# Optimization experiments

Hardware: AMD Instinct MI355X
Metric: run time of the kernel (lower is better)

## Reference

```python
import jax, jax.numpy as jnp
import numpy as np

N_SPK, M_UTT, D_EMB = 8192, 10, 128
CLAMP_MIN = 1e-6


def setup_inputs() -> dict:
    key = jax.random.key(0)
    x = jax.random.normal(key, (N_SPK, M_UTT, D_EMB), dtype=jnp.float32)
    w = jnp.asarray(10.0, dtype=jnp.float32)   # learned scale (init_w)
    b = jnp.asarray(-5.0, dtype=jnp.float32)   # learned bias  (init_b)
    return {"x": x, "w": w, "b": b}


def reference(x, w, b):
    # x: [N, M, D]. Faithful to the torch module:
    #   - centroids = mean over all M utterances per speaker
    #   - calc_new_centroids replaces speaker's own centroid with mean(dvecs[spkr,:M]),
    #     which IS the full centroid -> new_centroids == centroids (no-op, kept faithful)
    #   - only the last utterance (utt_indx == M-1) contributes a row -> [N, 1, N]
    n, m, d = x.shape
    centroids = jnp.mean(x, axis=1)                       # [N, D]
    last = x[:, m - 1, :]                                 # [N, D] last utterance per speaker
    num = jnp.einsum('nd,kd->nk', last, centroids)        # [N, N]
    denom = (jnp.linalg.norm(last, axis=1)[:, None]
             * jnp.linalg.norm(centroids, axis=1)[None, :])
    cos_sim = jnp.clip(num / denom, CLAMP_MIN)            # torch.clamp(x, 1e-6) = min-clamp
    logits = cos_sim * w + b                              # [N, N] (view(-1, N) with M=1)
    # CrossEntropyLoss with labels arange(N) (repeat_interleave with M=1 is identity)
    logp = jax.nn.log_softmax(logits, axis=-1)
    labels = jnp.arange(n)
    loss = -jnp.mean(jnp.take_along_axis(logp, labels[:, None], axis=1))
    return loss
```

## Files before the change

### kernel.cpp

```cpp
#include <hip/hip_runtime.h>
#include <hip/hip_bf16.h>


typedef __attribute__((ext_vector_type(8))) short short8;
typedef __attribute__((ext_vector_type(4))) float f32x4;

#define NSPK 8192
#define DEMB 128
#define MUTT 10
#define LOG2E 1.44269504088896340736f
#define LN2   0.69314718055994530942f

#define WS_ZDIAG 0
#define WS_ZSUM  8192
#define WS_LASTB 65536
#define WS_CENTB 2162688

__global__ __launch_bounds__(256) void k1_prep(const float* __restrict__ x,
                                               const float* __restrict__ wp,
                                               float* __restrict__ W,
                                               __hip_bfloat16* __restrict__ lastb,
                                               __hip_bfloat16* __restrict__ centb) {
    const int wv = threadIdx.x >> 6;
    const int l  = threadIdx.x & 63;
    const int n  = blockIdx.x * 4 + wv;
    if (blockIdx.x < 32) W[WS_ZSUM + blockIdx.x * 256 + threadIdx.x] = 0.f;

    const float* xr = x + (size_t)n * (MUTT * DEMB) + 2 * l;
    float sx = 0.f, sy = 0.f, vx = 0.f, vy = 0.f;
#pragma unroll
    for (int m = 0; m < MUTT; ++m) {
        float2 t = *(const float2*)(xr + m * DEMB);
        vx = t.x; vy = t.y; sx += t.x; sy += t.y;
    }
    const float cx = sx * 0.1f, cy = sy * 0.1f;
    float sl = vx * vx + vy * vy;
    float sc = cx * cx + cy * cy;
    float dp = vx * cx + vy * cy;
#pragma unroll
    for (int off = 1; off < 64; off <<= 1) {
        sl += __shfl_xor(sl, off);
        sc += __shfl_xor(sc, off);
        dp += __shfl_xor(dp, off);
    }
    const float il = rsqrtf(sl), ic = rsqrtf(sc);
    const float scale = wp[0] * LOG2E;
    const float as = il * scale;
    __hip_bfloat162 lv, cv;
    lv.x = __float2bfloat16(vx * as); lv.y = __float2bfloat16(vy * as);
    cv.x = __float2bfloat16(cx * ic); cv.y = __float2bfloat16(cy * ic);
    *(__hip_bfloat162*)(lastb + n * DEMB + 2 * l) = lv;
    *(__hip_bfloat162*)(centb + n * DEMB + 2 * l) = cv;
    if (l == 0) {
        const float lo = scale >= 0.f ? 1e-6f * scale : -INFINITY;
        const float hi = scale >= 0.f ? INFINITY : 1e-6f * scale;
        W[WS_ZDIAG + n] = fminf(fmaxf(dp * il * ic * scale, lo), hi);
    }
}

__global__ __launch_bounds__(256, 2) void k2_main(
        const __hip_bfloat16* __restrict__ lastb,
        const __hip_bfloat16* __restrict__ centb,
        const float* __restrict__ wp,
        float* __restrict__ W) {
    const int tid  = threadIdx.x;
    const int lane = tid & 63;
    const int wv   = tid >> 6;
    const int quad = lane >> 4;
    const int l16  = lane & 15;
    const int R0   = blockIdx.x * 256;
    const int C0   = blockIdx.y * 512;
    const float scale = wp[0] * LOG2E;
    const float lo = scale >= 0.f ? 1e-6f * scale : -INFINITY;
    const float hi = scale >= 0.f ? INFINITY : 1e-6f * scale;

    __shared__ uint4 Bs4[1024];
    char* Bsc = (char*)Bs4;

    short8 a[4][4];
    {
        const short* ap = (const short*)lastb + (size_t)(R0 + wv * 64 + l16) * DEMB + quad * 8;
#pragma unroll
        for (int rt = 0; rt < 4; ++rt)
#pragma unroll
            for (int kc = 0; kc < 4; ++kc)
                a[rt][kc] = *(const short8*)(ap + rt * 16 * DEMB + kc * 32);
    }

    int roff[4];
#pragma unroll
    for (int kc = 0; kc < 4; ++kc)
        roff[kc] = l16 * 256 + (((quad + 4 * kc) ^ l16) << 4);

    const int srow = wv * 16 + (lane >> 4);
    const int sp   = lane & 15;
    float racc[4][4] = {{0.f}};

    for (int it = 0; it < 8; ++it) {
        const int c0 = C0 + it * 64;
        __syncthreads();
#pragma unroll
        for (int i = 0; i < 4; ++i) {
            const int row = srow + i * 4;
            const int c   = sp ^ (row & 15);
            const char* src = (const char*)centb + ((size_t)(c0 + row) << 8) + (c << 4);
            char* dst = Bsc + (wv * 4096 + i * 1024 + lane * 16);
            __builtin_amdgcn_global_load_lds(
                (const __attribute__((address_space(1))) unsigned int*)src,
                (__attribute__((address_space(3))) unsigned int*)dst, 16, 0, 0);
        }
        __syncthreads();
#pragma unroll
        for (int nt = 0; nt < 4; ++nt) {
            short8 b[4];
#pragma unroll
            for (int kc = 0; kc < 4; ++kc)
                b[kc] = *(const short8*)(Bsc + nt * 4096 + roff[kc]);
#pragma unroll
            for (int rt = 0; rt < 4; ++rt) {
                f32x4 acc = {0.f, 0.f, 0.f, 0.f};
#pragma unroll
                for (int kc = 0; kc < 4; ++kc)
                    acc = __builtin_amdgcn_mfma_f32_16x16x32_bf16(a[rt][kc], b[kc], acc, 0, 0, 0);
#pragma unroll
                for (int r = 0; r < 4; ++r) {
                    const float z = fminf(fmaxf(acc[r], lo), hi);
                    racc[rt][r] += exp2f(z);
                }
            }
        }
    }
#pragma unroll
    for (int off = 1; off < 16; off <<= 1)
#pragma unroll
        for (int rt = 0; rt < 4; ++rt)
#pragma unroll
            for (int r = 0; r < 4; ++r)
                racc[rt][r] += __shfl_xor(racc[rt][r], off);
    if (l16 == 0) {
#pragma unroll
        for (int rt = 0; rt < 4; ++rt)
#pragma unroll
            for (int r = 0; r < 4; ++r)
                atomicAdd(&W[WS_ZSUM + R0 + wv * 64 + rt * 16 + quad * 4 + r], racc[rt][r]);
    }
}

__global__ __launch_bounds__(256) void k3_loss(const float* __restrict__ W,
                                               float* __restrict__ out) {
    float v = 0.f;
    for (int n = threadIdx.x; n < NSPK; n += 256)
        v += __log2f(W[WS_ZSUM + n]) - W[WS_ZDIAG + n];
#pragma unroll
    for (int off = 1; off < 64; off <<= 1) v += __shfl_xor(v, off);
    __shared__ float red[4];
    if ((threadIdx.x & 63) == 0) red[threadIdx.x >> 6] = v;
    __syncthreads();
    if (threadIdx.x == 0)
        out[0] = (red[0] + red[1] + red[2] + red[3]) * (LN2 / (float)NSPK);
}

extern "C" void kernel_launch(void* const* d_in, const int* in_sizes, int n_in,
                              void* d_out, int out_size, void* d_ws, size_t ws_size,
                              hipStream_t stream) {
    const float* x = (const float*)d_in[0];
    const float* w = (const float*)d_in[1];
    float* W = (float*)d_ws;
    __hip_bfloat16* lastb = (__hip_bfloat16*)((char*)d_ws + WS_LASTB);
    __hip_bfloat16* centb = (__hip_bfloat16*)((char*)d_ws + WS_CENTB);

    k1_prep<<<NSPK / 4, 256, 0, stream>>>(x, w, W, lastb, centb);
    k2_main<<<dim3(32, 16), 256, 0, stream>>>(lastb, centb, w, W);
    k3_loss<<<1, 256, 0, stream>>>(W, (float*)d_out);
}
```

Baseline: 123.2 us.

## Double-buffer centroid LDS tiles and clamp after hardware exp2

Centroid tiles are now double-buffered in LDS. The next 64-row tile is fetched with global_load_lds while the MFMA and exp work runs on the current buffer, and the second barrier per iteration is gone. The clamp on the logit moves after the exponential and is applied to the exponentiated bounds, which is equivalent because exp2 is monotone. This lets the raw hardware exp2 intrinsic replace the library exp2f and its range-handling code. LDS use doubles to 32 KB per block, and correctness relies on the barrier waiting for the outstanding async LDS loads.

Measured after the change: 114.6 us. 1.08x faster.

```diff
diff --git a/kernel.cpp b/kernel.cpp
--- a/kernel.cpp
+++ b/kernel.cpp
@@ -71,11 +71,26 @@
     const int R0   = blockIdx.x * 256;
     const int C0   = blockIdx.y * 512;
     const float scale = wp[0] * LOG2E;
-    const float lo = scale >= 0.f ? 1e-6f * scale : -INFINITY;
-    const float hi = scale >= 0.f ? INFINITY : 1e-6f * scale;
+    const float c0  = __builtin_amdgcn_exp2f(1e-6f * scale);
+    const float elo = scale >= 0.f ? c0 : 0.f;
+    const float ehi = scale >= 0.f ? INFINITY : c0;
 
-    __shared__ uint4 Bs4[1024];
+    __shared__ uint4 Bs4[2048];
     char* Bsc = (char*)Bs4;
+
+    const int srow = wv * 16 + quad;
+    const int sp   = l16;
+
+#pragma unroll
+    for (int i = 0; i < 4; ++i) {
+        const int row = srow + i * 4;
+        const int c   = sp ^ (row & 15);
+        const char* src = (const char*)centb + ((size_t)(C0 + row) << 8) + (c << 4);
+        char* dst = Bsc + (wv * 4096 + i * 1024 + lane * 16);
+        __builtin_amdgcn_global_load_lds(
+            (const __attribute__((address_space(1))) unsigned int*)src,
+            (__attribute__((address_space(3))) unsigned int*)dst, 16, 0, 0);
+    }
 
     short8 a[4][4];
     {
@@ -92,30 +107,31 @@
     for (int kc = 0; kc < 4; ++kc)
         roff[kc] = l16 * 256 + (((quad + 4 * kc) ^ l16) << 4);
 
-    const int srow = wv * 16 + (lane >> 4);
-    const int sp   = lane & 15;
     float racc[4][4] = {{0.f}};
 
     for (int it = 0; it < 8; ++it) {
-        const int c0 = C0 + it * 64;
         __syncthreads();
+        if (it < 7) {
+            const int c0n = C0 + (it + 1) * 64;
+            char* bufn = Bsc + ((it + 1) & 1) * 16384;
 #pragma unroll
-        for (int i = 0; i < 4; ++i) {
-            const int row = srow + i * 4;
-            const int c   = sp ^ (row & 15);
-            const char* src = (const char*)centb + ((size_t)(c0 + row) << 8) + (c << 4);
-            char* dst = Bsc + (wv * 4096 + i * 1024 + lane * 16);
-            __builtin_amdgcn_global_load_lds(
-                (const __attribute__((address_space(1))) unsigned int*)src,
-                (__attribute__((address_space(3))) unsigned int*)dst, 16, 0, 0);
+            for (int i = 0; i < 4; ++i) {
+                const int row = srow + i * 4;
+                const int c   = sp ^ (row & 15);
+                const char* src = (const char*)centb + ((size_t)(c0n + row) << 8) + (c << 4);
+                char* dst = bufn + (wv * 4096 + i * 1024 + lane * 16);
+                __builtin_amdgcn_global_load_lds(
+                    (const __attribute__((address_space(1))) unsigned int*)src,
+                    (__attribute__((address_space(3))) unsigned int*)dst, 16, 0, 0);
+            }
         }
-        __syncthreads();
+        const char* buf = Bsc + (it & 1) * 16384;
 #pragma unroll
         for (int nt = 0; nt < 4; ++nt) {
             short8 b[4];
 #pragma unroll
             for (int kc = 0; kc < 4; ++kc)
-                b[kc] = *(const short8*)(Bsc + nt * 4096 + roff[kc]);
+                b[kc] = *(const short8*)(buf + nt * 4096 + roff[kc]);
 #pragma unroll
             for (int rt = 0; rt < 4; ++rt) {
                 f32x4 acc = {0.f, 0.f, 0.f, 0.f};
@@ -124,8 +140,8 @@
                     acc = __builtin_amdgcn_mfma_f32_16x16x32_bf16(a[rt][kc], b[kc], acc, 0, 0, 0);
 #pragma unroll
                 for (int r = 0; r < 4; ++r) {
-                    const float z = fminf(fmaxf(acc[r], lo), hi);
-                    racc[rt][r] += exp2f(z);
+                    const float e = __builtin_amdgcn_exp2f(acc[r]);
+                    racc[rt][r] += fminf(fmaxf(e, elo), ehi);
                 }
             }
         }
```

## Load centroid tiles directly into registers and replace atomics with partial sums

Applied to the files above, without the earlier changes.

The main kernel stops staging centroid tiles in LDS. Each wave now loads its B fragments straight from global memory into double-buffered registers, which removes the barriers and LDS traffic. The grid doubles along columns to 32 chunks of 256, occupancy is raised to 3 blocks per SM, and exp2f is replaced by the hardware exp2 builtin. Per-chunk row sums are written to a partial buffer instead of atomically added, so the zeroing step disappears, but the single-block loss kernel must now sum 32 partials per row, and centroid reads are no longer shared across waves within a block.

Result: slower. 187.7 us (+52.3%).

```diff
diff --git a/kernel.cpp b/kernel.cpp
--- a/kernel.cpp
+++ b/kernel.cpp
@@ -10,11 +10,12 @@
 #define MUTT 10
 #define LOG2E 1.44269504088896340736f
 #define LN2   0.69314718055994530942f
+#define NCHUNK 32
 
 #define WS_ZDIAG 0
-#define WS_ZSUM  8192
-#define WS_LASTB 65536
-#define WS_CENTB 2162688
+#define WS_SPART 8192
+#define WS_LASTB 1114112
+#define WS_CENTB 3211264
 
 __global__ __launch_bounds__(256) void k1_prep(const float* __restrict__ x,
                                                const float* __restrict__ wp,
@@ -24,7 +25,6 @@
     const int wv = threadIdx.x >> 6;
     const int l  = threadIdx.x & 63;
     const int n  = blockIdx.x * 4 + wv;
-    if (blockIdx.x < 32) W[WS_ZSUM + blockIdx.x * 256 + threadIdx.x] = 0.f;
 
     const float* xr = x + (size_t)n * (MUTT * DEMB) + 2 * l;
     float sx = 0.f, sy = 0.f, vx = 0.f, vy = 0.f;
@@ -58,7 +58,7 @@
     }
 }
 
-__global__ __launch_bounds__(256, 2) void k2_main(
+__global__ __launch_bounds__(256, 3) void k2_main(
         const __hip_bfloat16* __restrict__ lastb,
         const __hip_bfloat16* __restrict__ centb,
         const float* __restrict__ wp,
@@ -69,13 +69,10 @@
     const int quad = lane >> 4;
     const int l16  = lane & 15;
     const int R0   = blockIdx.x * 256;
-    const int C0   = blockIdx.y * 512;
+    const int C0   = blockIdx.y * 256;
     const float scale = wp[0] * LOG2E;
     const float lo = scale >= 0.f ? 1e-6f * scale : -INFINITY;
     const float hi = scale >= 0.f ? INFINITY : 1e-6f * scale;
-
-    __shared__ uint4 Bs4[1024];
-    char* Bsc = (char*)Bs4;
 
     short8 a[4][4];
     {
@@ -87,46 +84,35 @@
                 a[rt][kc] = *(const short8*)(ap + rt * 16 * DEMB + kc * 32);
     }
 
-    int roff[4];
+    const char* cb = (const char*)centb;
+    const size_t bbase = ((size_t)(C0 + l16) << 8) + (quad << 4);
+
+    short8 b0[4], b1[4];
 #pragma unroll
     for (int kc = 0; kc < 4; ++kc)
-        roff[kc] = l16 * 256 + (((quad + 4 * kc) ^ l16) << 4);
+        b0[kc] = *(const short8*)(cb + bbase + kc * 64);
 
-    const int srow = wv * 16 + (lane >> 4);
-    const int sp   = lane & 15;
     float racc[4][4] = {{0.f}};
 
-    for (int it = 0; it < 8; ++it) {
-        const int c0 = C0 + it * 64;
-        __syncthreads();
 #pragma unroll
-        for (int i = 0; i < 4; ++i) {
-            const int row = srow + i * 4;
-            const int c   = sp ^ (row & 15);
-            const char* src = (const char*)centb + ((size_t)(c0 + row) << 8) + (c << 4);
-            char* dst = Bsc + (wv * 4096 + i * 1024 + lane * 16);
-            __builtin_amdgcn_global_load_lds(
-                (const __attribute__((address_space(1))) unsigned int*)src,
-                (__attribute__((address_space(3))) unsigned int*)dst, 16, 0, 0);
-        }
-        __syncthreads();
-#pragma unroll
-        for (int nt = 0; nt < 4; ++nt) {
-            short8 b[4];
+    for (int s = 0; s < 16; ++s) {
+        const short8* bc = (s & 1) ? b1 : b0;
+        short8*       bn = (s & 1) ? b0 : b1;
+        if (s < 15) {
 #pragma unroll
             for (int kc = 0; kc < 4; ++kc)
-                b[kc] = *(const short8*)(Bsc + nt * 4096 + roff[kc]);
+                bn[kc] = *(const short8*)(cb + bbase + (size_t)(s + 1) * 4096 + kc * 64);
+        }
 #pragma unroll
-            for (int rt = 0; rt < 4; ++rt) {
-                f32x4 acc = {0.f, 0.f, 0.f, 0.f};
+        for (int rt = 0; rt < 4; ++rt) {
+            f32x4 acc = {0.f, 0.f, 0.f, 0.f};
 #pragma unroll
-                for (int kc = 0; kc < 4; ++kc)
-                    acc = __builtin_amdgcn_mfma_f32_16x16x32_bf16(a[rt][kc], b[kc], acc, 0, 0, 0);
+            for (int kc = 0; kc < 4; ++kc)
+                acc = __builtin_amdgcn_mfma_f32_16x16x32_bf16(a[rt][kc], bc[kc], acc, 0, 0, 0);
 #pragma unroll
-                for (int r = 0; r < 4; ++r) {
-                    const float z = fminf(fmaxf(acc[r], lo), hi);
-                    racc[rt][r] += exp2f(z);
-                }
+            for (int r = 0; r < 4; ++r) {
+                const float z = fminf(fmaxf(acc[r], lo), hi);
+                racc[rt][r] += __builtin_amdgcn_exp2f(z);
             }
         }
     }
@@ -142,15 +128,20 @@
         for (int rt = 0; rt < 4; ++rt)
 #pragma unroll
             for (int r = 0; r < 4; ++r)
-                atomicAdd(&W[WS_ZSUM + R0 + wv * 64 + rt * 16 + quad * 4 + r], racc[rt][r]);
+                W[WS_SPART + blockIdx.y * NSPK + R0 + wv * 64 + rt * 16 + quad * 4 + r]
+                    = racc[rt][r];
     }
 }
 
 __global__ __launch_bounds__(256) void k3_loss(const float* __restrict__ W,
                                                float* __restrict__ out) {
     float v = 0.f;
-    for (int n = threadIdx.x; n < NSPK; n += 256)
-        v += __log2f(W[WS_ZSUM + n]) - W[WS_ZDIAG + n];
+    for (int n = threadIdx.x; n < NSPK; n += 256) {
+        float S = 0.f;
+#pragma unroll
+        for (int c = 0; c < NCHUNK; ++c) S += W[WS_SPART + c * NSPK + n];
+        v += __log2f(S) - W[WS_ZDIAG + n];
+    }
 #pragma unroll
     for (int off = 1; off < 64; off <<= 1) v += __shfl_xor(v, off);
     __shared__ float red[4];
@@ -170,6 +161,6 @@
     __hip_bfloat16* centb = (__hip_bfloat16*)((char*)d_ws + WS_CENTB);
 
     k1_prep<<<NSPK / 4, 256, 0, stream>>>(x, w, W, lastb, centb);
-    k2_main<<<dim3(32, 16), 256, 0, stream>>>(lastb, centb, w, W);
+    k2_main<<<dim3(32, 32), 256, 0, stream>>>(lastb, centb, w, W);
     k3_loss<<<1, 256, 0, stream>>>(W, (float*)d_out);
 }
```
